# Performance work log

Hardware: AMD Instinct MI355X
Metric: run time of the kernel (lower is better)

## Reference

```python
import jax, jax.numpy as jnp
import numpy as np

B, S, D, H = 2, 2048, 1024, 16
DEPTH = D // H
NEG = -1e9


def setup_inputs() -> dict:
    key = jax.random.key(0)
    ks = jax.random.split(key, 8)
    scale = 1.0 / np.sqrt(D)
    inp = {
        "query": jax.random.normal(ks[0], (B, S, D), jnp.float32),
        "key": jax.random.normal(ks[1], (B, S, D), jnp.float32),
        "value": jax.random.normal(ks[2], (B, S, D), jnp.float32),
        # causal look-ahead mask: 1 where attention is disallowed
        "mask": (1.0 - jnp.tril(jnp.ones((S, S), jnp.float32)))[None, None, :, :],
        "Wq": jax.random.normal(ks[3], (D, D), jnp.float32) * scale,
        "Wk": jax.random.normal(ks[4], (D, D), jnp.float32) * scale,
        "Wv": jax.random.normal(ks[5], (D, D), jnp.float32) * scale,
        "Wo": jax.random.normal(ks[6], (D, D), jnp.float32) * scale,
        "bq": jnp.zeros((D,), jnp.float32),
        "bk": jnp.zeros((D,), jnp.float32),
        "bv": jnp.zeros((D,), jnp.float32),
        "bo": jnp.zeros((D,), jnp.float32),
    }
    return inp


def _split_heads(x):
    # [B,S,D] -> [B,H,S,depth]
    return x.reshape(B, -1, H, DEPTH).transpose(0, 2, 1, 3)


def reference(query, key, value, mask, Wq, Wk, Wv, Wo, bq, bk, bv, bo):
    q = _split_heads(query @ Wq + bq)
    k = _split_heads(key @ Wk + bk)
    v = _split_heads(value @ Wv + bv)
    logits = jnp.einsum("bhqd,bhkd->bhqk", q, k) / jnp.sqrt(jnp.float32(DEPTH))
    logits = logits + mask * NEG
    attn = jax.nn.softmax(logits, axis=-1)
    ctx = jnp.einsum("bhqk,bhkd->bhqd", attn, v)  # [B,H,S,depth]
    concat = ctx.transpose(0, 2, 1, 3).reshape(B, -1, D)
    return concat @ Wo + bo
```

## Files before the change

kernel.cpp:

```cpp
#include <hip/hip_runtime.h>
#include <hip/hip_bf16.h>
#include <stdint.h>

#define BB 2
#define SS 2048
#define DDIM 1024
#define HH 16
#define DEPTH 64
#define MROWS (BB*SS)

typedef short bf16x8 __attribute__((ext_vector_type(8)));
typedef float f32x4 __attribute__((ext_vector_type(4)));

__device__ inline ushort f2bf(float f) {
  union { float f; unsigned u; } v; v.f = f;
  unsigned r = v.u + 0x7fffu + ((v.u >> 16) & 1u);
  return (ushort)(r >> 16);
}

__device__ inline uint pkbf(float a, float b) {
  uint r;
  asm("v_cvt_pk_bf16_f32 %0, %1, %2" : "=v"(r) : "v"(a), "v"(b));
  return r;
}

__device__ inline void gload_lds16(const void* g, void* l) {
  __builtin_amdgcn_global_load_lds(
      (const __attribute__((address_space(1))) unsigned*)g,
      (__attribute__((address_space(3))) unsigned*)l,
      16, 0, 0);
}

__global__ void wprep_kernel(const float* __restrict__ W0, const float* __restrict__ W1,
                             const float* __restrict__ W2, const float* __restrict__ W3,
                             ushort* __restrict__ T0, ushort* __restrict__ T1,
                             ushort* __restrict__ T2, ushort* __restrict__ T3) {
  __shared__ float tile[32][33];
  int z = blockIdx.x >> 10;
  int rr = blockIdx.x & 1023;
  const float* W = (z == 0) ? W0 : (z == 1) ? W1 : (z == 2) ? W2 : W3;
  ushort* T = (z == 0) ? T0 : (z == 1) ? T1 : (z == 2) ? T2 : T3;
  int tx = threadIdx.x & 31, ty = threadIdx.x >> 5;
  int n0 = (rr & 31) * 32, k0 = (rr >> 5) * 32;
#pragma unroll
  for (int i = 0; i < 4; i++)
    tile[ty + i * 8][tx] = W[(size_t)(k0 + ty + i * 8) * DDIM + n0 + tx];
  __syncthreads();
#pragma unroll
  for (int i = 0; i < 4; i++)
    T[(size_t)(n0 + ty + i * 8) * DDIM + k0 + tx] = f2bf(tile[tx][ty + i * 8]);
}

__global__ __launch_bounds__(256, 3) void qkv_gemm_kernel(
    const float* __restrict__ Aq, const float* __restrict__ Ak, const float* __restrict__ Av,
    const ushort* __restrict__ Wqt, const ushort* __restrict__ Wkt, const ushort* __restrict__ Wvt,
    const float* __restrict__ bqp, const float* __restrict__ bkp, const float* __restrict__ bvp,
    ushort* __restrict__ Qh, ushort* __restrict__ Kh, ushort* __restrict__ Vtg) {
  const int id = blockIdx.x;
  const int xcd = id & 7;
  const int rest = id >> 3;
  const int xblk = rest & 7;
  const int slot = rest >> 3;
  const int g = xcd * 12 + slot;
  const int yblk = g & 31;
  const int z = g >> 5;

  const float*  Ap = (z == 0) ? Aq  : (z == 1) ? Ak  : Av;
  const ushort* Bt = (z == 0) ? Wqt : (z == 1) ? Wkt : Wvt;
  const float* bias = (z == 0) ? bqp : (z == 1) ? bkp : bvp;

  __shared__ __align__(16) ushort As[128 * 64];
  __shared__ __align__(16) ushort Bs[2][128 * 64];
  const int tid = threadIdx.x;
  const int w = tid >> 6, lane = tid & 63;
  const int m0 = yblk * 128, n0 = xblk * 128;
  const int wr = (w >> 1) * 64, wc = (w & 1) * 64;
  const int l4 = lane >> 4, l15 = lane & 15;
  const int row16 = tid >> 4;
  const int col4 = (tid & 15) * 4;
  const int srow8 = w * 8 + (lane >> 3);
  const int scol8 = (lane & 7) * 8;

  f32x4 zero = {0.f, 0.f, 0.f, 0.f};
  f32x4 acc[4][4];
#pragma unroll
  for (int i = 0; i < 4; i++)
#pragma unroll
    for (int j = 0; j < 4; j++) acc[i][j] = zero;

  float4 areg[8];
#pragma unroll
  for (int j = 0; j < 8; ++j)
    areg[j] = *(const float4*)&Ap[(size_t)(m0 + j * 16 + row16) * DDIM + col4];
#pragma unroll
  for (int it = 0; it < 4; ++it)
    gload_lds16(Bt + (size_t)(n0 + it * 32 + srow8) * DDIM + scol8,
                &Bs[0][(it * 32 + w * 8) * 64]);
#pragma unroll
  for (int j = 0; j < 8; ++j) {
    uint2 pk;
    pk.x = pkbf(areg[j].x, areg[j].y);
    pk.y = pkbf(areg[j].z, areg[j].w);
    *(uint2*)&As[(j * 16 + row16) * 64 + col4] = pk;
  }
  __syncthreads();

  int buf = 0;
  for (int t = 0; t < 16; ++t) {
    if (t + 1 < 16) {
#pragma unroll
      for (int it = 0; it < 4; ++it)
        gload_lds16(Bt + (size_t)(n0 + it * 32 + srow8) * DDIM + (t + 1) * 64 + scol8,
                    &Bs[buf ^ 1][(it * 32 + w * 8) * 64]);
#pragma unroll
      for (int j = 0; j < 8; ++j)
        areg[j] = *(const float4*)&Ap[(size_t)(m0 + j * 16 + row16) * DDIM + (t + 1) * 64 + col4];
    }
#pragma unroll
    for (int kk = 0; kk < 2; ++kk) {
      bf16x8 af[4], bfr[4];
#pragma unroll
      for (int m = 0; m < 4; m++)
        af[m] = *(const bf16x8*)&As[(wr + m * 16 + l15) * 64 + kk * 32 + l4 * 8];
#pragma unroll
      for (int n = 0; n < 4; n++)
        bfr[n] = *(const bf16x8*)&Bs[buf][(wc + n * 16 + l15) * 64 + kk * 32 + l4 * 8];
#pragma unroll
      for (int m = 0; m < 4; m++)
#pragma unroll
        for (int n = 0; n < 4; n++)
          acc[m][n] = __builtin_amdgcn_mfma_f32_16x16x32_bf16(af[m], bfr[n], acc[m][n], 0, 0, 0);
    }
    __syncthreads();
    if (t + 1 < 16) {
#pragma unroll
      for (int j = 0; j < 8; ++j) {
        uint2 pk;
        pk.x = pkbf(areg[j].x, areg[j].y);
        pk.y = pkbf(areg[j].z, areg[j].w);
        *(uint2*)&As[(j * 16 + row16) * 64 + col4] = pk;
      }
    }
    __syncthreads();
    buf ^= 1;
  }

  if (z != 2) {
    ushort* outp = (z == 0) ? Qh : Kh;
    ushort* wtile = (w < 2) ? &As[w * 4096] : &Bs[0][(w - 2) * 4096];
    const int gcol0 = n0 + wc;
    const int hh = gcol0 >> 6;
    const int bb = m0 >> 11;
    const int s0g = (m0 + wr) & (SS - 1);
#pragma unroll
    for (int m = 0; m < 4; m++) {
#pragma unroll
      for (int n = 0; n < 4; n++) {
        int dloc = n * 16 + l15;
        float bv = bias[gcol0 + dloc];
#pragma unroll
        for (int r = 0; r < 4; r++) {
          int sloc = m * 16 + l4 * 4 + r;
          wtile[sloc * 64 + (dloc ^ ((sloc & 7) << 3))] = f2bf(acc[m][n][r] + bv);
        }
      }
    }
#pragma unroll
    for (int i = 0; i < 8; ++i) {
      int srow = i * 8 + (lane >> 3);
      int dch = (lane & 7) * 8;
      bf16x8 val = *(const bf16x8*)&wtile[srow * 64 + (dch ^ ((srow & 7) << 3))];
      *(bf16x8*)&outp[((size_t)(bb * HH + hh) * SS + s0g + srow) * DEPTH + dch] = val;
    }
  } else {
    ushort* wtile = (w < 2) ? &As[w * 2048] : &Bs[0][(w - 2) * 2048];
    const int gcol0 = n0 + wc;
    const int hh = gcol0 >> 6;
    const int bb = m0 >> 11;
    const int s0g = (m0 + wr) & (SS - 1);
#pragma unroll
    for (int p = 0; p < 2; ++p) {
#pragma unroll
      for (int nn = 0; nn < 2; ++nn) {
        int n = p * 2 + nn;
        int dloc = nn * 16 + l15;
        float bv = bias[gcol0 + p * 32 + dloc];
#pragma unroll
        for (int m = 0; m < 4; m++) {
#pragma unroll
          for (int rr = 0; rr < 4; rr += 2) {
            int sloc = m * 16 + l4 * 4 + rr;
            int gg = (sloc >> 3) ^ (dloc & 7);
            uint pk = pkbf(acc[m][n][rr] + bv, acc[m][n][rr + 1] + bv);
            *(uint*)&wtile[dloc * 64 + gg * 8 + (sloc & 7)] = pk;
          }
        }
      }
      __syncthreads();
#pragma unroll
      for (int i = 0; i < 4; ++i) {
        int dloc = (lane >> 3) + i * 8;
        int gg = (lane & 7) ^ (dloc & 7);
        bf16x8 val = *(const bf16x8*)&wtile[dloc * 64 + gg * 8];
        int dglob = p * 32 + dloc;
        size_t addr = ((size_t)(bb * HH + hh) * DEPTH + dglob) * SS + s0g + (lane & 7) * 8;
        *(bf16x8*)&Vtg[addr] = val;
      }
      __syncthreads();
    }
  }
}

__global__ __launch_bounds__(256, 3) void out_gemm_kernel(
    const ushort* __restrict__ A, const ushort* __restrict__ Bt,
    const float* __restrict__ bias, float* __restrict__ out,
    int M, int N, int K) {
  __shared__ __align__(16) ushort As[2][128 * 64];
  __shared__ __align__(16) ushort Bs[2][64 * 64];
  const int id = blockIdx.x;
  const int xcd = id & 7;
  const int rest = id >> 3;
  const int xblk = rest & 15;
  const int slot = rest >> 4;
  const int yblk = xcd * 4 + slot;

  const int tid = threadIdx.x;
  const int w = tid >> 6, lane = tid & 63;
  const int m0 = yblk * 128, n0 = xblk * 64;
  const int wr = (w >> 1) * 64, wc = (w & 1) * 32;
  const int l4 = lane >> 4, l15 = lane & 15;
  const int srow8 = w * 8 + (lane >> 3);
  const int scol8 = (lane & 7) * 8;

  f32x4 zero = {0.f, 0.f, 0.f, 0.f};
  f32x4 acc[4][2];
#pragma unroll
  for (int i = 0; i < 4; i++)
#pragma unroll
    for (int j = 0; j < 2; j++) acc[i][j] = zero;

#pragma unroll
  for (int it = 0; it < 4; ++it)
    gload_lds16(A + (size_t)(m0 + it * 32 + srow8) * K + scol8,
                &As[0][(it * 32 + w * 8) * 64]);
#pragma unroll
  for (int it = 0; it < 2; ++it)
    gload_lds16(Bt + (size_t)(n0 + it * 32 + srow8) * K + scol8,
                &Bs[0][(it * 32 + w * 8) * 64]);
  __syncthreads();

  int buf = 0;
  for (int t = 0; t < 16; ++t) {
    if (t + 1 < 16) {
#pragma unroll
      for (int it = 0; it < 4; ++it)
        gload_lds16(A + (size_t)(m0 + it * 32 + srow8) * K + (t + 1) * 64 + scol8,
                    &As[buf ^ 1][(it * 32 + w * 8) * 64]);
#pragma unroll
      for (int it = 0; it < 2; ++it)
        gload_lds16(Bt + (size_t)(n0 + it * 32 + srow8) * K + (t + 1) * 64 + scol8,
                    &Bs[buf ^ 1][(it * 32 + w * 8) * 64]);
    }
#pragma unroll
    for (int kk = 0; kk < 2; ++kk) {
      bf16x8 af[4], bfr[2];
#pragma unroll
      for (int m = 0; m < 4; m++)
        af[m] = *(const bf16x8*)&As[buf][(wr + m * 16 + l15) * 64 + kk * 32 + l4 * 8];
#pragma unroll
      for (int n = 0; n < 2; n++)
        bfr[n] = *(const bf16x8*)&Bs[buf][(wc + n * 16 + l15) * 64 + kk * 32 + l4 * 8];
#pragma unroll
      for (int m = 0; m < 4; m++)
#pragma unroll
        for (int n = 0; n < 2; n++)
          acc[m][n] = __builtin_amdgcn_mfma_f32_16x16x32_bf16(af[m], bfr[n], acc[m][n], 0, 0, 0);
    }
    __syncthreads();
    buf ^= 1;
  }

#pragma unroll
  for (int m = 0; m < 4; m++) {
#pragma unroll
    for (int n = 0; n < 2; n++) {
      int col = n0 + wc + n * 16 + l15;
      float bv = bias[col];
#pragma unroll
      for (int r = 0; r < 4; r++) {
        int row = m0 + wr + m * 16 + l4 * 4 + r;
        out[(size_t)row * N + col] = acc[m][n][r] + bv;
      }
    }
  }
}

__global__ __launch_bounds__(256, 4) void attn_kernel(
    const ushort* __restrict__ Qh, const ushort* __restrict__ Kh,
    const ushort* __restrict__ Vt, ushort* __restrict__ ctx) {
  __shared__ __align__(16) ushort Ks[2][64 * 64];
  __shared__ __align__(16) ushort Vs[2][64 * 64];
  __shared__ __align__(16) ushort Ps[4][16 * 64];
  const int tid = threadIdx.x;
  const int w = tid >> 6, lane = tid & 63;
  const int l4 = lane >> 4, l15 = lane & 15;
  const float CE = 0.18033688f;

  const int xcd = blockIdx.x & 7;
  const int local = blockIdx.x >> 3;
  const int bh = xcd * 4 + (local & 3);
  const int chunk = 31 - (local >> 2);
  const int b = bh >> 4, h = bh & 15;
  const size_t qkbase = (size_t)bh * SS * DEPTH;
  const size_t vbase  = (size_t)bh * DEPTH * SS;

  const int srow_w = w * 8 + (lane >> 3);
  const int colb_lin = (lane & 7) * 16;
  const int swz_rd = (l15 & 7) << 3;

  const int q0 = chunk * 64 + w * 16;
  const int nt = chunk + 1;

  bf16x8 aq[2];
#pragma unroll
  for (int cc = 0; cc < 2; cc++)
    aq[cc] = *(const bf16x8*)&Qh[qkbase + (size_t)(q0 + l15) * DEPTH + cc * 32 + l4 * 8];

  f32x4 zero = {0.f, 0.f, 0.f, 0.f};
  f32x4 o[4];
  float m_run = -__builtin_inff(), l_run = 0.f;
#pragma unroll
  for (int d = 0; d < 4; d++) o[d] = zero;

  int buf = 0;
#pragma unroll
  for (int it = 0; it < 2; ++it) {
    int row = it * 32 + srow_w;
    int col_e = (colb_lin ^ ((row & 7) << 4)) >> 1;
    int ldsoff = it * 2048 + w * 512;
    gload_lds16(Kh + qkbase + (size_t)row * DEPTH + col_e, &Ks[0][ldsoff]);
    gload_lds16(Vt + vbase + (size_t)row * SS + col_e, &Vs[0][ldsoff]);
  }
  __syncthreads();

  for (int t = 0; t < nt; ++t) {
    if (t + 1 < nt) {
      const int kv1 = (t + 1) * 64;
#pragma unroll
      for (int it = 0; it < 2; ++it) {
        int row = it * 32 + srow_w;
        int col_e = (colb_lin ^ ((row & 7) << 4)) >> 1;
        int ldsoff = it * 2048 + w * 512;
        gload_lds16(Kh + qkbase + (size_t)(kv1 + row) * DEPTH + col_e, &Ks[buf ^ 1][ldsoff]);
        gload_lds16(Vt + vbase + (size_t)row * SS + kv1 + col_e, &Vs[buf ^ 1][ldsoff]);
      }
    }

    const int kv0 = t * 64;
    f32x4 s[4];
    __builtin_amdgcn_s_setprio(1);
#pragma unroll
    for (int n = 0; n < 4; n++) {
      f32x4 zacc = zero;
      int kr = n * 16 + l15;
#pragma unroll
      for (int cc = 0; cc < 2; cc++) {
        bf16x8 bk = *(const bf16x8*)&Ks[buf][kr * 64 + ((cc * 32 + l4 * 8) ^ swz_rd)];
        zacc = __builtin_amdgcn_mfma_f32_16x16x32_bf16(bk, aq[cc], zacc, 0, 0, 0);
      }
      s[n] = zacc;
    }
    __builtin_amdgcn_s_setprio(0);

    const int qg = q0 + l15;
    if (t == nt - 1) {
#pragma unroll
      for (int n = 0; n < 4; n++) {
        int kb = kv0 + n * 16 + l4 * 4;
#pragma unroll
        for (int r = 0; r < 4; r++)
          if (kb + r > qg) s[n][r] = -1e9f;
      }
    }

    float mx = -__builtin_inff();
#pragma unroll
    for (int n = 0; n < 4; n++)
      mx = fmaxf(mx, fmaxf(fmaxf(s[n][0], s[n][1]), fmaxf(s[n][2], s[n][3])));
    mx = fmaxf(mx, __shfl_xor(mx, 16));
    mx = fmaxf(mx, __shfl_xor(mx, 32));
    if (!__all(mx - m_run <= 44.36f)) {
      float mnew = fmaxf(m_run, mx);
      float alpha = exp2f((m_run - mnew) * CE);
      m_run = mnew;
      l_run *= alpha;
#pragma unroll
      for (int d = 0; d < 4; d++) o[d] *= alpha;
    }
    float mc = m_run * CE;
    float rs = 0.f;
#pragma unroll
    for (int n = 0; n < 4; n++)
#pragma unroll
      for (int r = 0; r < 4; r++) {
        float p = exp2f(s[n][r] * CE - mc);
        s[n][r] = p;
        rs += p;
      }
    l_run += rs;

    ushort* Pw = &Ps[w][0];
#pragma unroll
    for (int n = 0; n < 4; n++) {
      int col = (n * 16 + l4 * 4) ^ swz_rd;
      uint2 pk;
      pk.x = pkbf(s[n][0], s[n][1]);
      pk.y = pkbf(s[n][2], s[n][3]);
      *(uint2*)&Pw[l15 * 64 + col] = pk;
    }

    bf16x8 pa[2];
#pragma unroll
    for (int cc = 0; cc < 2; cc++)
      pa[cc] = *(const bf16x8*)&Pw[l15 * 64 + ((cc * 32 + l4 * 8) ^ swz_rd)];

    __builtin_amdgcn_s_setprio(1);
#pragma unroll
    for (int d = 0; d < 4; d++) {
      int dr = d * 16 + l15;
#pragma unroll
      for (int cc = 0; cc < 2; cc++) {
        bf16x8 av = *(const bf16x8*)&Vs[buf][dr * 64 + ((cc * 32 + l4 * 8) ^ swz_rd)];
        o[d] = __builtin_amdgcn_mfma_f32_16x16x32_bf16(av, pa[cc], o[d], 0, 0, 0);
      }
    }
    __builtin_amdgcn_s_setprio(0);

    __syncthreads();
    buf ^= 1;
  }

  float lv = l_run;
  lv += __shfl_xor(lv, 16);
  lv += __shfl_xor(lv, 32);
  float inv = 1.f / lv;
  size_t rowbase = ((size_t)(b * SS + q0 + l15)) * DDIM + h * DEPTH;
#pragma unroll
  for (int d = 0; d < 4; d++) {
    *(uint*)&ctx[rowbase + d * 16 + l4 * 4]     = pkbf(o[d][0] * inv, o[d][1] * inv);
    *(uint*)&ctx[rowbase + d * 16 + l4 * 4 + 2] = pkbf(o[d][2] * inv, o[d][3] * inv);
  }
}

extern "C" void kernel_launch(void* const* d_in, const int* in_sizes, int n_in,
                              void* d_out, int out_size, void* d_ws, size_t ws_size,
                              hipStream_t stream) {
  const float* query = (const float*)d_in[0];
  const float* key_  = (const float*)d_in[1];
  const float* value = (const float*)d_in[2];
  const float* Wq = (const float*)d_in[4];
  const float* Wk = (const float*)d_in[5];
  const float* Wv = (const float*)d_in[6];
  const float* Wo = (const float*)d_in[7];
  const float* bq = (const float*)d_in[8];
  const float* bk = (const float*)d_in[9];
  const float* bv = (const float*)d_in[10];
  const float* bo = (const float*)d_in[11];

  char* ws = (char*)d_ws;
  const size_t MB = 1u << 20;
  ushort* Wqt = (ushort*)(ws + 24 * MB);
  ushort* Wkt = (ushort*)(ws + 26 * MB);
  ushort* Wvt = (ushort*)(ws + 28 * MB);
  ushort* Wot = (ushort*)(ws + 30 * MB);
  ushort* Qh  = (ushort*)(ws + 32 * MB);
  ushort* Kh  = (ushort*)(ws + 40 * MB);
  ushort* Vtg = (ushort*)(ws + 48 * MB);
  ushort* Cb  = (ushort*)(ws + 56 * MB);

  wprep_kernel<<<4096, 256, 0, stream>>>(Wq, Wk, Wv, Wo, Wqt, Wkt, Wvt, Wot);

  qkv_gemm_kernel<<<768, 256, 0, stream>>>(
      query, key_, value, Wqt, Wkt, Wvt, bq, bk, bv, Qh, Kh, Vtg);

  attn_kernel<<<1024, 256, 0, stream>>>(Qh, Kh, Vtg, Cb);

  out_gemm_kernel<<<512, 256, 0, stream>>>(
      Cb, Wot, bo, (float*)d_out, MROWS, DDIM, DDIM);
}
```

Before: 116.8 us.

## Restructure QKV GEMM to BK=32 double-buffered A and B with swizzled LDS

The QKV projection GEMM main loop now uses a K-tile of 32 and double-buffers both the converted A tile and the B tile in LDS, so each step needs one barrier instead of two. A global loads are prefetched two steps ahead in registers. The weight-prep kernel writes the transposed Q/K/V weights with an XOR swizzle that matches the new LDS read pattern, which is meant to reduce bank conflicts. Halving the LDS footprint allows launch bounds of 4 blocks per CU instead of 3, at the cost of twice as many loop iterations and less MFMA work per barrier.

```diff
diff --git a/kernel.cpp b/kernel.cpp
--- a/kernel.cpp
+++ b/kernel.cpp
@@ -47,11 +47,14 @@
     tile[ty + i * 8][tx] = W[(size_t)(k0 + ty + i * 8) * DDIM + n0 + tx];
   __syncthreads();
 #pragma unroll
-  for (int i = 0; i < 4; i++)
-    T[(size_t)(n0 + ty + i * 8) * DDIM + k0 + tx] = f2bf(tile[tx][ty + i * 8]);
-}
-
-__global__ __launch_bounds__(256, 3) void qkv_gemm_kernel(
+  for (int i = 0; i < 4; i++) {
+    int n = n0 + ty + i * 8;
+    int col = (z < 3) ? (k0 + (tx ^ ((n & 3) << 3))) : (k0 + tx);
+    T[(size_t)n * DDIM + col] = f2bf(tile[tx][ty + i * 8]);
+  }
+}
+
+__global__ __launch_bounds__(256, 4) void qkv_gemm_kernel(
     const float* __restrict__ Aq, const float* __restrict__ Ak, const float* __restrict__ Av,
     const ushort* __restrict__ Wqt, const ushort* __restrict__ Wkt, const ushort* __restrict__ Wvt,
     const float* __restrict__ bqp, const float* __restrict__ bkp, const float* __restrict__ bvp,
@@ -69,17 +72,20 @@
   const ushort* Bt = (z == 0) ? Wqt : (z == 1) ? Wkt : Wvt;
   const float* bias = (z == 0) ? bqp : (z == 1) ? bkp : bvp;
 
-  __shared__ __align__(16) ushort As[128 * 64];
-  __shared__ __align__(16) ushort Bs[2][128 * 64];
+  __shared__ __align__(16) ushort As[2][128 * 32];
+  __shared__ __align__(16) ushort Bs[2][128 * 32];
   const int tid = threadIdx.x;
   const int w = tid >> 6, lane = tid & 63;
   const int m0 = yblk * 128, n0 = xblk * 128;
   const int wr = (w >> 1) * 64, wc = (w & 1) * 64;
   const int l4 = lane >> 4, l15 = lane & 15;
-  const int row16 = tid >> 4;
-  const int col4 = (tid & 15) * 4;
-  const int srow8 = w * 8 + (lane >> 3);
-  const int scol8 = (lane & 7) * 8;
+  const int swzf = (l15 & 3) << 3;
+  const int arow = tid & 127;
+  const int acg  = (tid >> 7) * 16;
+  const int aswz = (arow & 3) << 3;
+  const size_t abase = (size_t)(m0 + arow) * DDIM;
+  const int bsr = lane >> 2;
+  const int bsc = (lane & 3) * 8;
 
   f32x4 zero = {0.f, 0.f, 0.f, 0.f};
   f32x4 acc[4][4];
@@ -88,66 +94,66 @@
 #pragma unroll
     for (int j = 0; j < 4; j++) acc[i][j] = zero;
 
-  float4 areg[8];
-#pragma unroll
-  for (int j = 0; j < 8; ++j)
-    areg[j] = *(const float4*)&Ap[(size_t)(m0 + j * 16 + row16) * DDIM + col4];
-#pragma unroll
-  for (int it = 0; it < 4; ++it)
-    gload_lds16(Bt + (size_t)(n0 + it * 32 + srow8) * DDIM + scol8,
-                &Bs[0][(it * 32 + w * 8) * 64]);
-#pragma unroll
-  for (int j = 0; j < 8; ++j) {
-    uint2 pk;
-    pk.x = pkbf(areg[j].x, areg[j].y);
-    pk.y = pkbf(areg[j].z, areg[j].w);
-    *(uint2*)&As[(j * 16 + row16) * 64 + col4] = pk;
-  }
+  float4 areg[4];
+#pragma unroll
+  for (int j = 0; j < 4; ++j)
+    areg[j] = *(const float4*)&Ap[abase + acg + j * 4];
+#pragma unroll
+  for (int it = 0; it < 2; ++it)
+    gload_lds16(Bt + (size_t)(n0 + it * 64 + w * 16 + bsr) * DDIM + bsc,
+                &Bs[0][(it * 64 + w * 16) * 32]);
+  {
+    uint4 p0, p1;
+    p0.x = pkbf(areg[0].x, areg[0].y); p0.y = pkbf(areg[0].z, areg[0].w);
+    p0.z = pkbf(areg[1].x, areg[1].y); p0.w = pkbf(areg[1].z, areg[1].w);
+    p1.x = pkbf(areg[2].x, areg[2].y); p1.y = pkbf(areg[2].z, areg[2].w);
+    p1.z = pkbf(areg[3].x, areg[3].y); p1.w = pkbf(areg[3].z, areg[3].w);
+    *(uint4*)&As[0][arow * 32 + (acg ^ aswz)]       = p0;
+    *(uint4*)&As[0][arow * 32 + ((acg + 8) ^ aswz)] = p1;
+  }
+#pragma unroll
+  for (int j = 0; j < 4; ++j)
+    areg[j] = *(const float4*)&Ap[abase + 32 + acg + j * 4];
   __syncthreads();
 
-  int buf = 0;
-  for (int t = 0; t < 16; ++t) {
-    if (t + 1 < 16) {
-#pragma unroll
-      for (int it = 0; it < 4; ++it)
-        gload_lds16(Bt + (size_t)(n0 + it * 32 + srow8) * DDIM + (t + 1) * 64 + scol8,
-                    &Bs[buf ^ 1][(it * 32 + w * 8) * 64]);
-#pragma unroll
-      for (int j = 0; j < 8; ++j)
-        areg[j] = *(const float4*)&Ap[(size_t)(m0 + j * 16 + row16) * DDIM + (t + 1) * 64 + col4];
-    }
-#pragma unroll
-    for (int kk = 0; kk < 2; ++kk) {
-      bf16x8 af[4], bfr[4];
-#pragma unroll
-      for (int m = 0; m < 4; m++)
-        af[m] = *(const bf16x8*)&As[(wr + m * 16 + l15) * 64 + kk * 32 + l4 * 8];
-#pragma unroll
-      for (int n = 0; n < 4; n++)
-        bfr[n] = *(const bf16x8*)&Bs[buf][(wc + n * 16 + l15) * 64 + kk * 32 + l4 * 8];
-#pragma unroll
-      for (int m = 0; m < 4; m++)
-#pragma unroll
-        for (int n = 0; n < 4; n++)
-          acc[m][n] = __builtin_amdgcn_mfma_f32_16x16x32_bf16(af[m], bfr[n], acc[m][n], 0, 0, 0);
+  int b = 0;
+  for (int t = 0; t < 32; ++t) {
+    if (t < 31) {
+#pragma unroll
+      for (int it = 0; it < 2; ++it)
+        gload_lds16(Bt + (size_t)(n0 + it * 64 + w * 16 + bsr) * DDIM + (t + 1) * 32 + bsc,
+                    &Bs[b ^ 1][(it * 64 + w * 16) * 32]);
+      uint4 p0, p1;
+      p0.x = pkbf(areg[0].x, areg[0].y); p0.y = pkbf(areg[0].z, areg[0].w);
+      p0.z = pkbf(areg[1].x, areg[1].y); p0.w = pkbf(areg[1].z, areg[1].w);
+      p1.x = pkbf(areg[2].x, areg[2].y); p1.y = pkbf(areg[2].z, areg[2].w);
+      p1.z = pkbf(areg[3].x, areg[3].y); p1.w = pkbf(areg[3].z, areg[3].w);
+      *(uint4*)&As[b ^ 1][arow * 32 + (acg ^ aswz)]       = p0;
+      *(uint4*)&As[b ^ 1][arow * 32 + ((acg + 8) ^ aswz)] = p1;
+      if (t < 30) {
+#pragma unroll
+        for (int j = 0; j < 4; ++j)
+          areg[j] = *(const float4*)&Ap[abase + (t + 2) * 32 + acg + j * 4];
+      }
+    }
+    bf16x8 bfr[4];
+#pragma unroll
+    for (int n = 0; n < 4; ++n)
+      bfr[n] = *(const bf16x8*)&Bs[b][(wc + n * 16 + l15) * 32 + ((l4 * 8) ^ swzf)];
+#pragma unroll
+    for (int m = 0; m < 4; ++m) {
+      bf16x8 af = *(const bf16x8*)&As[b][(wr + m * 16 + l15) * 32 + ((l4 * 8) ^ swzf)];
+#pragma unroll
+      for (int n = 0; n < 4; ++n)
+        acc[m][n] = __builtin_amdgcn_mfma_f32_16x16x32_bf16(af, bfr[n], acc[m][n], 0, 0, 0);
     }
     __syncthreads();
-    if (t + 1 < 16) {
-#pragma unroll
-      for (int j = 0; j < 8; ++j) {
-        uint2 pk;
-        pk.x = pkbf(areg[j].x, areg[j].y);
-        pk.y = pkbf(areg[j].z, areg[j].w);
-        *(uint2*)&As[(j * 16 + row16) * 64 + col4] = pk;
-      }
-    }
-    __syncthreads();
-    buf ^= 1;
+    b ^= 1;
   }
 
   if (z != 2) {
     ushort* outp = (z == 0) ? Qh : Kh;
-    ushort* wtile = (w < 2) ? &As[w * 4096] : &Bs[0][(w - 2) * 4096];
+    ushort* wtile = (w < 2) ? &As[w][0] : &Bs[w - 2][0];
     const int gcol0 = n0 + wc;
     const int hh = gcol0 >> 6;
     const int bb = m0 >> 11;
@@ -173,7 +179,7 @@
       *(bf16x8*)&outp[((size_t)(bb * HH + hh) * SS + s0g + srow) * DEPTH + dch] = val;
     }
   } else {
-    ushort* wtile = (w < 2) ? &As[w * 2048] : &Bs[0][(w - 2) * 2048];
+    ushort* wtile = (w < 2) ? &As[w][0] : &Bs[w - 2][0];
     const int gcol0 = n0 + wc;
     const int hh = gcol0 >> 6;
     const int bb = m0 >> 11;
```

New measurement: 134.3 us. 1.15x slower.
